# Optimization experiments

Measured on AMD Instinct MI355X. Metric: run time of the kernel, lower is better.

Reference implementation:

```python
import jax, jax.numpy as jnp
import numpy as np

HIDDEN = 2048
NUM_HEADS = 16
HEAD_DIM = HIDDEN // NUM_HEADS
ROPE_THETA = 10000.0


def rope_tables(T, dim, base):
    inv_freq = 1.0 / (base ** (jnp.arange(0, dim, 2, dtype=jnp.float32) / dim))
    t = jnp.arange(T, dtype=jnp.float32)
    freqs = jnp.outer(t, inv_freq)              # [T, dim/2]
    emb = jnp.concatenate([freqs, freqs], -1)   # [T, dim]
    return jnp.cos(emb), jnp.sin(emb)


def rotate_half(x):
    x1, x2 = jnp.split(x, 2, axis=-1)
    return jnp.concatenate([-x2, x1], axis=-1)


def setup_inputs() -> dict:
    key = jax.random.key(0)
    ks = jax.random.split(key, 5)
    B, T, C = 2, 2048, HIDDEN
    s = 1.0 / np.sqrt(C)
    return {
        "x": jax.random.normal(ks[0], (B, T, C), jnp.float32),
        "Wq": jax.random.normal(ks[1], (C, C), jnp.float32) * s,
        "Wk": jax.random.normal(ks[2], (C, C), jnp.float32) * s,
        "Wv": jax.random.normal(ks[3], (C, C), jnp.float32) * s,
        "Wo": jax.random.normal(ks[4], (C, C), jnp.float32) * s,
    }


def reference(x, Wq, Wk, Wv, Wo):
    B, T, C = x.shape
    H, D = NUM_HEADS, HEAD_DIM
    scale = D ** -0.5

    # projections (torch Linear: y = x @ W.T)
    q = (x @ Wq.T).reshape(B, T, H, D).transpose(0, 2, 1, 3)  # [B,H,T,D]
    k = (x @ Wk.T).reshape(B, T, H, D).transpose(0, 2, 1, 3)
    v = (x @ Wv.T).reshape(B, T, H, D).transpose(0, 2, 1, 3)

    cos, sin = rope_tables(T, D, ROPE_THETA)  # [T, D]
    cos = cos[None, None, :, :]
    sin = sin[None, None, :, :]
    q = q * cos + rotate_half(q) * sin
    k = k * cos + rotate_half(k) * sin

    scores = jnp.einsum("bhqd,bhkd->bhqk", q, k) * scale
    causal = jnp.tril(jnp.ones((T, T), dtype=bool))
    scores = jnp.where(causal, scores, -jnp.inf)
    probs = jax.nn.softmax(scores, axis=-1)
    out = jnp.einsum("bhqk,bhkd->bhqd", probs, v)
    out = out.transpose(0, 2, 1, 3).reshape(B, T, C)
    return out @ Wo.T
```

## Files before the change

kernel.cpp:

```cpp
#include <hip/hip_runtime.h>
#include <hip/hip_bf16.h>


typedef __attribute__((ext_vector_type(4))) float f32x4;
typedef __attribute__((ext_vector_type(8))) short s16x8;
typedef __attribute__((ext_vector_type(4))) short s16x4;

typedef void __attribute__((address_space(1))) gvoid;
typedef void __attribute__((address_space(3))) svoid;
#define ASYNC16(ldsp, gp) __builtin_amdgcn_global_load_lds((gvoid*)(gp), (svoid*)(ldsp), 16, 0, 0)

__device__ __forceinline__ float bf2f(short b) {
  unsigned u = ((unsigned)(unsigned short)b) << 16;
  float f; __builtin_memcpy(&f, &u, 4); return f;
}
__device__ __forceinline__ short f2bf(float f) {
  unsigned u; __builtin_memcpy(&u, &f, 4);
  u += 0x7FFFu + ((u >> 16) & 1u);
  return (short)(u >> 16);
}

__device__ __forceinline__ f32x4 mfma16(s16x8 a, s16x8 b, f32x4 c) {
  return __builtin_amdgcn_mfma_f32_16x16x32_bf16(a, b, c, 0, 0, 0);
}

__global__ __launch_bounds__(256)
void cvt_k(const float* __restrict__ in, short* __restrict__ out, int n4) {
  int i = blockIdx.x * 256 + threadIdx.x;
  if (i < n4) {
    f32x4 v = *(const f32x4*)&in[i * 4];
    s16x4 o;
#pragma unroll
    for (int e = 0; e < 4; e++) o[e] = f2bf(v[e]);
    *(s16x4*)&out[i * 4] = o;
  }
}

__global__ __launch_bounds__(256)
void cvt_w4_k(const float* __restrict__ w0, const float* __restrict__ w1,
              const float* __restrict__ w2, const float* __restrict__ w3,
              short* __restrict__ o0, short* __restrict__ o1,
              short* __restrict__ o2, short* __restrict__ o3) {
  int i = blockIdx.x * 256 + threadIdx.x;
  int sel = i >> 20, j = i & 1048575;
  const float* in = (sel == 0) ? w0 : (sel == 1) ? w1 : (sel == 2) ? w2 : w3;
  short* out = (sel == 0) ? o0 : (sel == 1) ? o1 : (sel == 2) ? o2 : o3;
  f32x4 v = *(const f32x4*)&in[j * 4];
  s16x4 o;
#pragma unroll
  for (int e = 0; e < 4; e++) o[e] = f2bf(v[e]);
  *(s16x4*)&out[j * 4] = o;
}

__global__ void rope_tables_k(float* __restrict__ cosT, float* __restrict__ sinT) {
  int t = blockIdx.x, j = threadIdx.x;
  float inv = exp2f(-(float)j * 0.20762050593046f);
  float a = (float)t * inv;
  cosT[t * 64 + j] = cosf(a);
  sinT[t * 64 + j] = sinf(a);
}

__global__ __launch_bounds__(256)
void rope_apply_k(short* __restrict__ q, short* __restrict__ kk,
                  const float* __restrict__ cosT, const float* __restrict__ sinT) {
  int gid = blockIdx.x * 256 + threadIdx.x;
  int jb = (gid & 7) * 8;
  int h  = (gid >> 3) & 15;
  int row = gid >> 7;
  int t = row & 2047;
  long base = (long)row * 2048 + h * 128 + jb;
  float cc[8], ss[8];
  *(f32x4*)&cc[0] = *(const f32x4*)&cosT[t * 64 + jb];
  *(f32x4*)&cc[4] = *(const f32x4*)&cosT[t * 64 + jb + 4];
  *(f32x4*)&ss[0] = *(const f32x4*)&sinT[t * 64 + jb];
  *(f32x4*)&ss[4] = *(const f32x4*)&sinT[t * 64 + jb + 4];

  {
    s16x8 lo = *(s16x8*)&q[base];
    s16x8 hi = *(s16x8*)&q[base + 64];
    s16x8 nlo, nhi;
#pragma unroll
    for (int e = 0; e < 8; e++) {
      float a = bf2f(lo[e]), b = bf2f(hi[e]);
      nlo[e] = f2bf(a * cc[e] - b * ss[e]);
      nhi[e] = f2bf(b * cc[e] + a * ss[e]);
    }
    *(s16x8*)&q[base] = nlo;
    *(s16x8*)&q[base + 64] = nhi;
  }
  {
    s16x8 lo = *(s16x8*)&kk[base];
    s16x8 hi = *(s16x8*)&kk[base + 64];
    s16x8 nlo, nhi;
#pragma unroll
    for (int e = 0; e < 8; e++) {
      float a = bf2f(lo[e]), b = bf2f(hi[e]);
      nlo[e] = f2bf(a * cc[e] - b * ss[e]);
      nhi[e] = f2bf(b * cc[e] + a * ss[e]);
    }
    *(s16x8*)&kk[base] = nlo;
    *(s16x8*)&kk[base + 64] = nhi;
  }
}

__device__ __forceinline__ void store_out(float* p, float v) { *p = v; }
__device__ __forceinline__ void store_out(short* p, float v) { *p = f2bf(v); }

template <typename OutT>
__device__ __forceinline__ void gemm_tile(const short* A, const short* B,
                                          OutT* Cmat, int m0, int n0,
                                          int K, int ldc,
                                          short* As, short* Bs) {
  const int tid = threadIdx.x;
  const int wave = tid >> 6, lane = tid & 63;
  const int lr = lane & 15, lk = lane >> 4;
  const int wr = (wave >> 1) * 64, wc = (wave & 1) * 64;

  f32x4 acc[4][4] = {};

  const int srow = tid >> 2;
  const int scol = (tid & 3) * 8;
  const short* aptr0 = A + (long)(m0 + srow) * K + scol;
  const short* aptr1 = A + (long)(m0 + 64 + srow) * K + scol;
  const short* bptr0 = B + (long)(srow) * K + scol;
  const short* bptr1 = B + (long)(64 + srow) * K + scol;

  for (int kt = 0; kt < K; kt += 32) {
    __syncthreads();
    ASYNC16(&As[tid * 8],        aptr0 + kt);
    ASYNC16(&As[2048 + tid * 8], aptr1 + kt);
    ASYNC16(&Bs[tid * 8],        bptr0 + kt);
    ASYNC16(&Bs[2048 + tid * 8], bptr1 + kt);
    __syncthreads();
    s16x8 af[4], bfr[4];
#pragma unroll
    for (int i = 0; i < 4; i++)
      af[i] = *(const s16x8*)&As[(wr + i * 16 + lr) * 32 + lk * 8];
#pragma unroll
    for (int i = 0; i < 4; i++)
      bfr[i] = *(const s16x8*)&Bs[(wc + i * 16 + lr) * 32 + lk * 8];
#pragma unroll
    for (int mi = 0; mi < 4; mi++)
#pragma unroll
      for (int ni = 0; ni < 4; ni++)
        acc[mi][ni] = mfma16(af[mi], bfr[ni], acc[mi][ni]);
  }
#pragma unroll
  for (int mi = 0; mi < 4; mi++)
#pragma unroll
    for (int ni = 0; ni < 4; ni++)
#pragma unroll
      for (int r = 0; r < 4; r++) {
        int row = m0 + wr + mi * 16 + lk * 4 + r;
        int col = n0 + wc + ni * 16 + lr;
        store_out(&Cmat[(long)row * ldc + col], acc[mi][ni][r]);
      }
}

__global__ __launch_bounds__(256)
void gemm_qkv_k(const short* __restrict__ A,
                const short* __restrict__ Bq, const short* __restrict__ Bk,
                const short* __restrict__ Bv,
                short* __restrict__ Cq, short* __restrict__ Ck,
                short* __restrict__ Cv, int K) {
  __shared__ short As[128 * 32];
  __shared__ short Bs[128 * 32];
  int nblk = blockIdx.x;
  int sel = nblk >> 4;
  int ncol = (nblk & 15) * 128;
  const short* B = (sel == 0) ? Bq : (sel == 1) ? Bk : Bv;
  short* C = (sel == 0) ? Cq : (sel == 1) ? Ck : Cv;
  gemm_tile<short>(A, B + (long)ncol * K, C, blockIdx.y * 128, ncol, K, 2048, As, Bs);
}

__global__ __launch_bounds__(256)
void gemm_out_k(const short* __restrict__ A, const short* __restrict__ B,
                float* __restrict__ C, int K) {
  __shared__ short As[128 * 32];
  __shared__ short Bs[128 * 32];
  gemm_tile<float>(A, B + (long)(blockIdx.x * 128) * K, C,
                   blockIdx.y * 128, blockIdx.x * 128, K, 2048, As, Bs);
}

__global__ __launch_bounds__(256)
void attn_k(const short* __restrict__ q, const short* __restrict__ k,
            const short* __restrict__ v, short* __restrict__ o) {
  __shared__ short Ks[2][64 * 128];
  __shared__ short Vt[128 * 72];
  __shared__ short Pl[4][16 * 72];
  const int tid = threadIdx.x;
  const int wave = tid >> 6, lane = tid & 63;
  const int lr = lane & 15, lq = lane >> 4;
  const int h = blockIdx.y, b = blockIdx.z;
  const long rowb = (long)b * 2048;
  const int hoff = h * 128;
  const float scale = 0.08838834764831845f;

  const int vr = (tid & 31) * 2;
  const int vcol = (tid >> 5) * 16;

  for (int pass = 0; pass < 2; pass++) {
    const int qt = pass ? (31 - blockIdx.x) : blockIdx.x;
    const int qbase = qt * 64;
    const int nt = qt + 1;

    s16x8 qf[4];
    {
      const short* qp = q + (rowb + qbase + wave * 16 + lr) * 2048 + hoff + lq * 8;
#pragma unroll
      for (int ks = 0; ks < 4; ks++) qf[ks] = *(const s16x8*)(qp + ks * 32);
    }
    f32x4 acc[8] = {};
    float mrun[4], lrun[4];
#pragma unroll
    for (int r = 0; r < 4; r++) { mrun[r] = -1e30f; lrun[r] = 0.f; }

    s16x8 vl[4];
    {
      const short* vp = v + (rowb + vr) * 2048 + hoff + vcol;
      vl[0] = *(const s16x8*)vp;       vl[1] = *(const s16x8*)(vp + 8);
      vl[2] = *(const s16x8*)(vp + 2048); vl[3] = *(const s16x8*)(vp + 2048 + 8);
    }
#pragma unroll
    for (int L = 0; L < 4; L++) {
      int ci = L * 256 + tid;
      int krow = ci >> 4, dslot = ci & 15;
      int col = (dslot ^ (krow & 7)) * 8;
      ASYNC16(&Ks[0][ci * 8], k + (rowb + krow) * 2048 + hoff + col);
    }
#pragma unroll
    for (int e = 0; e < 16; e++) {
      int col = vcol + e;
      unsigned pk = (unsigned)(unsigned short)vl[e >> 3][e & 7]
                  | ((unsigned)(unsigned short)vl[2 + (e >> 3)][e & 7] << 16);
      *(unsigned*)&Vt[col * 72 + vr] = pk;
    }
    __syncthreads();

    int cur = 0;
    for (int ti = 0; ti < nt; ti++) {
      const int kv0 = ti * 64;
      const bool pre = (ti + 1 < nt);
      s16x8 vn[4];
      if (pre) {
        const short* vp = v + (rowb + kv0 + 64 + vr) * 2048 + hoff + vcol;
        vn[0] = *(const s16x8*)vp;       vn[1] = *(const s16x8*)(vp + 8);
        vn[2] = *(const s16x8*)(vp + 2048); vn[3] = *(const s16x8*)(vp + 2048 + 8);
#pragma unroll
        for (int L = 0; L < 4; L++) {
          int ci = L * 256 + tid;
          int krow = ci >> 4, dslot = ci & 15;
          int col = (dslot ^ (krow & 7)) * 8;
          ASYNC16(&Ks[cur ^ 1][ci * 8], k + (rowb + kv0 + 64 + krow) * 2048 + hoff + col);
        }
      }
      f32x4 s[4] = {};
#pragma unroll
      for (int kvf = 0; kvf < 4; kvf++) {
        const int krow = kvf * 16 + lr;
#pragma unroll
        for (int ks = 0; ks < 4; ks++) {
          int doff = ks * 4 + lq;
          s16x8 kf = *(const s16x8*)&Ks[cur][krow * 128 + ((doff ^ (krow & 7)) * 8)];
          s[kvf] = mfma16(qf[ks], kf, s[kvf]);
        }
      }
#pragma unroll
      for (int kvf = 0; kvf < 4; kvf++)
#pragma unroll
        for (int r = 0; r < 4; r++) s[kvf][r] *= scale;
      if (ti == nt - 1) {
#pragma unroll
        for (int kvf = 0; kvf < 4; kvf++) {
          int kvc = kv0 + kvf * 16 + lr;
#pragma unroll
          for (int r = 0; r < 4; r++) {
            int qr = qbase + wave * 16 + lq * 4 + r;
            if (kvc > qr) s[kvf][r] = -3.0e38f;
          }
        }
      }
      float mt[4], rs[4];
#pragma unroll
      for (int r = 0; r < 4; r++)
        mt[r] = fmaxf(fmaxf(s[0][r], s[1][r]), fmaxf(s[2][r], s[3][r]));
#pragma unroll
      for (int d = 1; d < 16; d <<= 1)
#pragma unroll
        for (int r = 0; r < 4; r++) mt[r] = fmaxf(mt[r], __shfl_xor(mt[r], d));
      int need = 0;
#pragma unroll
      for (int r = 0; r < 4; r++) need |= (mt[r] > mrun[r] + 8.f);
      if (__any(need)) {
#pragma unroll
        for (int r = 0; r < 4; r++) {
          float mn = fmaxf(mrun[r], mt[r]);
          float sf = __expf(mrun[r] - mn);
          mrun[r] = mn;
          lrun[r] *= sf;
#pragma unroll
          for (int df = 0; df < 8; df++) acc[df][r] *= sf;
        }
      }
      short* pw = &Pl[wave][0];
#pragma unroll
      for (int r = 0; r < 4; r++) rs[r] = 0.f;
#pragma unroll
      for (int kvf = 0; kvf < 4; kvf++)
#pragma unroll
        for (int r = 0; r < 4; r++) {
          float p = __expf(s[kvf][r] - mrun[r]);
          rs[r] += p;
          pw[(lq * 4 + r) * 72 + kvf * 16 + lr] = f2bf(p);
        }
#pragma unroll
      for (int d = 1; d < 16; d <<= 1)
#pragma unroll
        for (int r = 0; r < 4; r++) rs[r] += __shfl_xor(rs[r], d);
#pragma unroll
      for (int r = 0; r < 4; r++) lrun[r] += rs[r];
      s16x8 pf0 = *(const s16x8*)&pw[lr * 72 + lq * 8];
      s16x8 pf1 = *(const s16x8*)&pw[lr * 72 + 32 + lq * 8];
#pragma unroll
      for (int df = 0; df < 8; df++) {
        s16x8 vf0 = *(const s16x8*)&Vt[(df * 16 + lr) * 72 + lq * 8];
        s16x8 vf1 = *(const s16x8*)&Vt[(df * 16 + lr) * 72 + 32 + lq * 8];
        acc[df] = mfma16(pf0, vf0, acc[df]);
        acc[df] = mfma16(pf1, vf1, acc[df]);
      }
      __syncthreads();
      if (pre) {
#pragma unroll
        for (int e = 0; e < 16; e++) {
          int col = vcol + e;
          unsigned pk = (unsigned)(unsigned short)vn[e >> 3][e & 7]
                      | ((unsigned)(unsigned short)vn[2 + (e >> 3)][e & 7] << 16);
          *(unsigned*)&Vt[col * 72 + vr] = pk;
        }
        __syncthreads();
      }
      cur ^= 1;
    }
#pragma unroll
    for (int r = 0; r < 4; r++) {
      float inv = 1.0f / lrun[r];
      long orow = rowb + qbase + wave * 16 + lq * 4 + r;
#pragma unroll
      for (int df = 0; df < 8; df++)
        o[orow * 2048 + hoff + df * 16 + lr] = f2bf(acc[df][r] * inv);
    }
  }
}

extern "C" void kernel_launch(void* const* d_in, const int* in_sizes, int n_in,
                              void* d_out, int out_size, void* d_ws, size_t ws_size,
                              hipStream_t stream) {
  const float* x  = (const float*)d_in[0];
  const float* Wq = (const float*)d_in[1];
  const float* Wk = (const float*)d_in[2];
  const float* Wv = (const float*)d_in[3];
  const float* Wo = (const float*)d_in[4];
  float* out = (float*)d_out;

  char* p = (char*)d_ws;
  short* xb  = (short*)p; p += 8388608L * 2;
  short* wqb = (short*)p; p += 4194304L * 2;
  short* wkb = (short*)p; p += 4194304L * 2;
  short* wvb = (short*)p; p += 4194304L * 2;
  short* wob = (short*)p; p += 4194304L * 2;
  short* qb  = (short*)p; p += 8388608L * 2;
  short* kb  = (short*)p; p += 8388608L * 2;
  short* vb  = (short*)p; p += 8388608L * 2;
  short* ab  = (short*)p; p += 8388608L * 2;
  float* cosT = (float*)p; p += 131072L * 4;
  float* sinT = (float*)p; p += 131072L * 4;

  cvt_k<<<8192, 256, 0, stream>>>(x, xb, 2097152);
  cvt_w4_k<<<16384, 256, 0, stream>>>(Wq, Wk, Wv, Wo, wqb, wkb, wvb, wob);
  rope_tables_k<<<2048, 64, 0, stream>>>(cosT, sinT);

  gemm_qkv_k<<<dim3(48, 32), 256, 0, stream>>>(xb, wqb, wkb, wvb, qb, kb, vb, 2048);

  rope_apply_k<<<2048, 256, 0, stream>>>(qb, kb, cosT, sinT);

  attn_k<<<dim3(16, 16, 2), 256, 0, stream>>>(qb, kb, vb, ab);

  gemm_out_k<<<dim3(16, 32), 256, 0, stream>>>(ab, wob, out, 2048);
}
```

Baseline: 444.4 us.

## Replace GEMMs with 256x256 double-buffered swizzled LDS pipeline

Replaces the 128x128, BK=32 GEMM tile with a 256x256, BK=64 tile using 8 waves. LDS is double-buffered with async global-to-LDS loads interleaved between MFMA phases, and accesses are XOR-swizzled to avoid bank conflicts. Wave priority is raised during MFMA bursts. This increases data reuse and overlaps memory with compute, at the cost of 128KB LDS per block and fewer blocks, which underfills CUs for the output projection.

```diff
diff --git a/kernel.cpp b/kernel.cpp
--- a/kernel.cpp
+++ b/kernel.cpp
@@ -106,80 +106,143 @@
 __device__ __forceinline__ void store_out(float* p, float v) { *p = v; }
 __device__ __forceinline__ void store_out(short* p, float v) { *p = f2bf(v); }
 
+
+#define STAGE_A(Abase, buf, h, t)                                              \
+  { ASYNC16(&As[(buf)*16384 + (h)*8192 + lin0*8],                              \
+            (Abase) + (long)(m0 + (h)*128 + r0) * K + (t)*64 + kk0);           \
+    ASYNC16(&As[(buf)*16384 + (h)*8192 + lin1*8],                              \
+            (Abase) + (long)(m0 + (h)*128 + r1) * K + (t)*64 + kk1); }
+#define STAGE_B(Bbase, buf, h, t)                                              \
+  { ASYNC16(&Bs[(buf)*16384 + (h)*8192 + lin0*8],                              \
+            (Bbase) + (long)((h)*128 + r0) * K + (t)*64 + kk0);                \
+    ASYNC16(&Bs[(buf)*16384 + (h)*8192 + lin1*8],                              \
+            (Bbase) + (long)((h)*128 + r1) * K + (t)*64 + kk1); }
+#define LDA(mi, ks) (*(const s16x8*)&As[p*16384 +                              \
+    (wr*128 + (mi)*16 + lr)*64 + (((ks)*4 + lk) ^ (lr & 7))*8])
+#define LDB(ni, ks) (*(const s16x8*)&Bs[p*16384 +                              \
+    (wc*64 + (ni)*16 + lr)*64 + (((ks)*4 + lk) ^ (lr & 7))*8])
+
 template <typename OutT>
-__device__ __forceinline__ void gemm_tile(const short* A, const short* B,
-                                          OutT* Cmat, int m0, int n0,
-                                          int K, int ldc,
-                                          short* As, short* Bs) {
+__device__ __forceinline__ void gemm8_tile(const short* __restrict__ A,
+                                           const short* __restrict__ B,
+                                           OutT* __restrict__ Cmat,
+                                           int n0, int K, int ldc,
+                                           short* As, short* Bs) {
   const int tid = threadIdx.x;
-  const int wave = tid >> 6, lane = tid & 63;
+  const int wid = tid >> 6, lane = tid & 63;
   const int lr = lane & 15, lk = lane >> 4;
-  const int wr = (wave >> 1) * 64, wc = (wave & 1) * 64;
-
-  f32x4 acc[4][4] = {};
-
-  const int srow = tid >> 2;
-  const int scol = (tid & 3) * 8;
-  const short* aptr0 = A + (long)(m0 + srow) * K + scol;
-  const short* aptr1 = A + (long)(m0 + 64 + srow) * K + scol;
-  const short* bptr0 = B + (long)(srow) * K + scol;
-  const short* bptr1 = B + (long)(64 + srow) * K + scol;
-
-  for (int kt = 0; kt < K; kt += 32) {
-    __syncthreads();
-    ASYNC16(&As[tid * 8],        aptr0 + kt);
-    ASYNC16(&As[2048 + tid * 8], aptr1 + kt);
-    ASYNC16(&Bs[tid * 8],        bptr0 + kt);
-    ASYNC16(&Bs[2048 + tid * 8], bptr1 + kt);
-    __syncthreads();
-    s16x8 af[4], bfr[4];
-#pragma unroll
-    for (int i = 0; i < 4; i++)
-      af[i] = *(const s16x8*)&As[(wr + i * 16 + lr) * 32 + lk * 8];
-#pragma unroll
-    for (int i = 0; i < 4; i++)
-      bfr[i] = *(const s16x8*)&Bs[(wc + i * 16 + lr) * 32 + lk * 8];
-#pragma unroll
-    for (int mi = 0; mi < 4; mi++)
-#pragma unroll
-      for (int ni = 0; ni < 4; ni++)
-        acc[mi][ni] = mfma16(af[mi], bfr[ni], acc[mi][ni]);
+  const int wr = wid >> 2, wc = wid & 3;
+  const int m0 = blockIdx.y * 256;
+
+  const int lin0 = wid * 128 + lane;
+  const int lin1 = wid * 128 + 64 + lane;
+  const int r0 = lin0 >> 3, r1 = lin1 >> 3;
+  const int kk0 = ((lin0 & 7) ^ (r0 & 7)) * 8;
+  const int kk1 = ((lin1 & 7) ^ (r1 & 7)) * 8;
+
+  f32x4 acc[8][4] = {};
+  const int NT = K >> 6;
+
+  STAGE_A(A, 0, 0, 0); STAGE_A(A, 0, 1, 0);
+  STAGE_B(B, 0, 0, 0); STAGE_B(B, 0, 1, 0);
+  STAGE_A(A, 1, 0, 1);
+  asm volatile("s_waitcnt vmcnt(2)" ::: "memory");
+  __builtin_amdgcn_sched_barrier(0);
+  __builtin_amdgcn_s_barrier();
+
+  for (int t = 0; t < NT; ++t) {
+    const int p = t & 1;
+    const bool s1 = (t + 1 < NT), s2 = (t + 2 < NT);
+    s16x8 af[8], b0, b1;
+#pragma unroll
+    for (int mi = 0; mi < 8; mi++) af[mi] = LDA(mi, 0);
+    b0 = LDB(0, 0); b1 = LDB(1, 0);
+    if (s1) STAGE_A(A, p ^ 1, 1, t + 1);
+    __builtin_amdgcn_s_barrier();
+    __builtin_amdgcn_s_setprio(1);
+#pragma unroll
+    for (int mi = 0; mi < 8; mi++) {
+      acc[mi][0] = mfma16(af[mi], b0, acc[mi][0]);
+      acc[mi][1] = mfma16(af[mi], b1, acc[mi][1]);
+    }
+    __builtin_amdgcn_s_setprio(0);
+    __builtin_amdgcn_s_barrier();
+    b0 = LDB(2, 0); b1 = LDB(3, 0);
+    if (s1) STAGE_B(B, p ^ 1, 0, t + 1);
+    __builtin_amdgcn_s_barrier();
+    __builtin_amdgcn_s_setprio(1);
+#pragma unroll
+    for (int mi = 0; mi < 8; mi++) {
+      acc[mi][2] = mfma16(af[mi], b0, acc[mi][2]);
+      acc[mi][3] = mfma16(af[mi], b1, acc[mi][3]);
+    }
+    __builtin_amdgcn_s_setprio(0);
+    __builtin_amdgcn_s_barrier();
+#pragma unroll
+    for (int mi = 0; mi < 8; mi++) af[mi] = LDA(mi, 1);
+    b0 = LDB(0, 1); b1 = LDB(1, 1);
+    if (s1) STAGE_B(B, p ^ 1, 1, t + 1);
+    __builtin_amdgcn_s_barrier();
+    __builtin_amdgcn_s_setprio(1);
+#pragma unroll
+    for (int mi = 0; mi < 8; mi++) {
+      acc[mi][0] = mfma16(af[mi], b0, acc[mi][0]);
+      acc[mi][1] = mfma16(af[mi], b1, acc[mi][1]);
+    }
+    __builtin_amdgcn_s_setprio(0);
+    __builtin_amdgcn_s_barrier();
+    b0 = LDB(2, 1); b1 = LDB(3, 1);
+    if (s2) {
+      STAGE_A(A, p, 0, t + 2);
+      asm volatile("s_waitcnt vmcnt(2)" ::: "memory");
+    } else {
+      asm volatile("s_waitcnt vmcnt(0)" ::: "memory");
+    }
+    __builtin_amdgcn_sched_barrier(0);
+    __builtin_amdgcn_s_barrier();
+    __builtin_amdgcn_s_setprio(1);
+#pragma unroll
+    for (int mi = 0; mi < 8; mi++) {
+      acc[mi][2] = mfma16(af[mi], b0, acc[mi][2]);
+      acc[mi][3] = mfma16(af[mi], b1, acc[mi][3]);
+    }
+    __builtin_amdgcn_s_setprio(0);
+    __builtin_amdgcn_s_barrier();
   }
 #pragma unroll
-  for (int mi = 0; mi < 4; mi++)
+  for (int mi = 0; mi < 8; mi++)
 #pragma unroll
     for (int ni = 0; ni < 4; ni++)
 #pragma unroll
       for (int r = 0; r < 4; r++) {
-        int row = m0 + wr + mi * 16 + lk * 4 + r;
-        int col = n0 + wc + ni * 16 + lr;
+        int row = m0 + wr * 128 + mi * 16 + lk * 4 + r;
+        int col = n0 + wc * 64 + ni * 16 + lr;
         store_out(&Cmat[(long)row * ldc + col], acc[mi][ni][r]);
       }
 }
 
-__global__ __launch_bounds__(256)
-void gemm_qkv_k(const short* __restrict__ A,
-                const short* __restrict__ Bq, const short* __restrict__ Bk,
-                const short* __restrict__ Bv,
-                short* __restrict__ Cq, short* __restrict__ Ck,
-                short* __restrict__ Cv, int K) {
-  __shared__ short As[128 * 32];
-  __shared__ short Bs[128 * 32];
-  int nblk = blockIdx.x;
-  int sel = nblk >> 4;
-  int ncol = (nblk & 15) * 128;
+__global__ __launch_bounds__(512, 2)
+void gemm8_qkv_k(const short* __restrict__ A,
+                 const short* __restrict__ Bq, const short* __restrict__ Bk,
+                 const short* __restrict__ Bv,
+                 short* __restrict__ Cq, short* __restrict__ Ck,
+                 short* __restrict__ Cv, int K) {
+  __shared__ short As[2 * 16384];
+  __shared__ short Bs[2 * 16384];
+  int sel = blockIdx.x >> 3;
+  int ncol = (blockIdx.x & 7) * 256;
   const short* B = (sel == 0) ? Bq : (sel == 1) ? Bk : Bv;
   short* C = (sel == 0) ? Cq : (sel == 1) ? Ck : Cv;
-  gemm_tile<short>(A, B + (long)ncol * K, C, blockIdx.y * 128, ncol, K, 2048, As, Bs);
-}
-
-__global__ __launch_bounds__(256)
-void gemm_out_k(const short* __restrict__ A, const short* __restrict__ B,
-                float* __restrict__ C, int K) {
-  __shared__ short As[128 * 32];
-  __shared__ short Bs[128 * 32];
-  gemm_tile<float>(A, B + (long)(blockIdx.x * 128) * K, C,
-                   blockIdx.y * 128, blockIdx.x * 128, K, 2048, As, Bs);
+  gemm8_tile<short>(A, B + (long)ncol * K, C, ncol, K, 2048, As, Bs);
+}
+
+__global__ __launch_bounds__(512, 2)
+void gemm8_out_k(const short* __restrict__ A, const short* __restrict__ B,
+                 float* __restrict__ C, int K) {
+  __shared__ short As[2 * 16384];
+  __shared__ short Bs[2 * 16384];
+  int ncol = blockIdx.x * 256;
+  gemm8_tile<float>(A, B + (long)ncol * K, C, ncol, K, 2048, As, Bs);
 }
 
 __global__ __launch_bounds__(256)
@@ -379,11 +442,11 @@
   cvt_w4_k<<<16384, 256, 0, stream>>>(Wq, Wk, Wv, Wo, wqb, wkb, wvb, wob);
   rope_tables_k<<<2048, 64, 0, stream>>>(cosT, sinT);
 
-  gemm_qkv_k<<<dim3(48, 32), 256, 0, stream>>>(xb, wqb, wkb, wvb, qb, kb, vb, 2048);
+  gemm8_qkv_k<<<dim3(24, 16), 512, 0, stream>>>(xb, wqb, wkb, wvb, qb, kb, vb, 2048);
 
   rope_apply_k<<<2048, 256, 0, stream>>>(qb, kb, cosT, sinT);
 
   attn_k<<<dim3(16, 16, 2), 256, 0, stream>>>(qb, kb, vb, ab);
 
-  gemm_out_k<<<dim3(16, 32), 256, 0, stream>>>(ab, wob, out, 2048);
-}
+  gemm8_out_k<<<dim3(8, 16), 512, 0, stream>>>(ab, wob, out, 2048);
+}
```

After: 434.1 us. -2.3%, faster.
